# Kernel optimization log

Measured on AMD Instinct MI355X. Metric: run time of the kernel, lower is better.

## Reference

```python
import jax, jax.numpy as jnp
import numpy as np

HEADS = 8


def setup_inputs() -> dict:
    key = jax.random.key(0)
    ks = jax.random.split(key, 18)
    B, L, D, N = 512, 70, 128, 100000
    r = lambda i, shape: jax.random.normal(ks[i], shape, dtype=jnp.float32) * 0.1
    return {
        "hidden": r(0, (B, L, D)),
        "hidden0": r(1, (B, L, D)),
        "mask": jnp.ones((B, L), dtype=jnp.int32),
        "s": r(2, (B, D)),
        "emb": r(3, (N, D)),
        "attn_in_w": r(4, (3 * D, D)),
        "attn_in_b": r(5, (3 * D,)),
        "attn_out_w": r(6, (D, D)),
        "attn_out_b": r(7, (D,)),
        "w_zero": r(8, (D, D)),
        "b_zero": r(9, (D,)),
        "w_one": r(10, (D, D)),
        "b_one": r(11, (D,)),
        "w_two": r(12, (D, D)),
        "b_two": r(13, (D,)),
        "w_three": r(14, (HEADS, D)),
        "w_gate": r(15, (1, 2 * D)),
        "w_trans": r(16, (D, 2 * D)),
        "b_trans": r(17, (D,)),
    }


def _mha(q, k, v, in_w, in_b, out_w, out_b, h):
    # torch.nn.MultiheadAttention, eval mode (dropout=0)
    B, Lq, D = q.shape
    Lk = k.shape[1]
    hd = D // h
    wq, wk, wv = jnp.split(in_w, 3, axis=0)
    bq, bk, bv = jnp.split(in_b, 3)
    qp = (q @ wq.T + bq).reshape(B, Lq, h, hd)
    kp = (k @ wk.T + bk).reshape(B, Lk, h, hd)
    vp = (v @ wv.T + bv).reshape(B, Lk, h, hd)
    scores = jnp.einsum("bqhd,bkhd->bhqk", qp, kp) / jnp.sqrt(jnp.float32(hd))
    w = jax.nn.softmax(scores, axis=-1)
    o = jnp.einsum("bhqk,bkhd->bqhd", w, vp).reshape(B, Lq, D)
    return o @ out_w.T + out_b


def reference(hidden, hidden0, mask, s, emb,
              attn_in_w, attn_in_b, attn_out_w, attn_out_b,
              w_zero, b_zero, w_one, b_one, w_two, b_two,
              w_three, w_gate, w_trans, b_trans):
    B, L, D = hidden.shape
    H = HEADS
    # last-item gather (last_k = 1)
    last_idx = jnp.clip(jnp.sum(mask, axis=1) - 1, 0, 1000)
    ht0 = hidden[jnp.arange(B), last_idx]  # [B, D]
    ht1 = ht0
    # attention of pooled session vector over item states
    ht = _mha(s[:, None, :], hidden, hidden,
              attn_in_w, attn_in_b, attn_out_w, attn_out_b, H)  # [B, 1, D]
    # sigmoid gated fusion of hidden0 / hidden
    sigma = jax.nn.sigmoid(jnp.concatenate([hidden0, hidden], axis=-1) @ w_gate.T)  # [B, L, 1]
    hidden = hidden0 * sigma + hidden * (1.0 - sigma)
    # additive multi-head attention scores
    q0 = (ht1 @ w_zero.T + b_zero)[:, None, :]          # [B, 1, D]
    q1 = ht @ w_one.T + b_one                           # [B, 1, D]
    q2 = hidden @ w_two.T + b_two                       # [B, L, D]
    alpha = jax.nn.sigmoid(q1 + q2 + q0) @ w_three.T    # [B, L, H]
    alpha = jnp.where((mask == 0)[:, :, None], -jnp.inf, alpha)
    alpha = jax.nn.softmax(alpha, axis=1)
    # head-split mask-weighted sum reduction
    mf = mask.astype(hidden.dtype)[:, :, None]
    a = jnp.sum((alpha[..., None] * hidden.reshape(B, L, H, D // H)).reshape(B, L, D) * mf, axis=1)  # [B, D]
    # hybrid transform with last item
    a = jnp.concatenate([a, ht0], axis=1) @ w_trans.T + b_trans
    # normalized scoring against item table (skipping padding idx 0)
    b = emb[1:]
    a = a / (jnp.linalg.norm(a, axis=1, keepdims=True) + 1e-12)
    b = b / (jnp.linalg.norm(b, axis=1, keepdims=True) + 1e-12)
    scores = 12.0 * (a @ b.T)  # [B, n_node-1]
    return scores
```

## Files before the change

### kernel.cpp

```cpp
#include <hip/hip_runtime.h>
#include <hip/hip_bf16.h>

#define B_SZ 512
#define L_SZ 70
#define D_SZ 128
#define NCOL 99999
#define M_ROWS (B_SZ * L_SZ)

typedef __attribute__((ext_vector_type(4))) float f32x4;
typedef __attribute__((ext_vector_type(8))) short bf16x8;

static __device__ __forceinline__ short f2bf(float x) {
    union { float f; unsigned u; } v; v.f = x;
    unsigned r = v.u + 0x7fffu + ((v.u >> 16) & 1u);
    return (short)(r >> 16);
}
static __device__ __forceinline__ float bf2f(unsigned short h) {
    union { unsigned u; float f; } v; v.u = ((unsigned)h) << 16; return v.f;
}

__global__ void k_prep_w(const float* attn_in_w, const float* w_two,
                         short* Wkv, short* W2) {
    int i = blockIdx.x * 256 + threadIdx.x;
    if (i < 256 * 128) Wkv[i] = f2bf(attn_in_w[128 * 128 + i]);
    if (i < 128 * 128) W2[i] = f2bf(w_two[i]);
}

__global__ void k_ht0_qp(const float* hidden, const int* mask, const float* s,
                         const float* attn_in_w, const float* attn_in_b,
                         float* ht0, float* qp) {
    int b = blockIdx.x, t = threadIdx.x;
    __shared__ float s_sh[128];
    __shared__ int idx_sh;
    if (t < 64) {
        int acc = 0;
        for (int l = t; l < L_SZ; l += 64) acc += mask[b * L_SZ + l];
        for (int off = 32; off; off >>= 1) acc += __shfl_down(acc, off);
        if (t == 0) {
            int idx = acc - 1;
            if (idx < 0) idx = 0;
            if (idx > L_SZ - 1) idx = L_SZ - 1;
            idx_sh = idx;
        }
    }
    s_sh[t] = s[b * 128 + t];
    __syncthreads();
    int idx = idx_sh;
    ht0[b * 128 + t] = hidden[(b * L_SZ + idx) * 128 + t];
    float acc = attn_in_b[t];
    const float* wq = attn_in_w + t * 128;
    for (int k = 0; k < 128; k++) acc += s_sh[k] * wq[k];
    qp[b * 128 + t] = acc;
}

__global__ void k_gate(const float* hidden, const float* hidden0,
                       const float* w_gate, short* g_bf) {
    int row = blockIdx.x, t = threadIdx.x;
    float h0 = hidden0[row * 128 + t], h = hidden[row * 128 + t];
    float p = h0 * w_gate[t] + h * w_gate[128 + t];
    for (int off = 32; off; off >>= 1) p += __shfl_down(p, off);
    __shared__ float part[2];
    __shared__ float sig_sh;
    if ((t & 63) == 0) part[t >> 6] = p;
    __syncthreads();
    if (t == 0) {
        float tot = part[0] + part[1];
        sig_sh = 1.f / (1.f + __expf(-tot));
    }
    __syncthreads();
    float sg = sig_sh;
    g_bf[row * 128 + t] = f2bf(h0 * sg + h * (1.f - sg));
}

__global__ void k_gemm_kv(const float* hidden, const short* Wkv,
                          const float* attn_in_b, short* kv) {
    int lane = threadIdx.x & 63, w = threadIdx.x >> 6;
    int r0 = blockIdx.x * 64 + w * 16;
    int ar = r0 + (lane & 15);
    int kbase = (lane >> 4) * 8;
    bf16x8 aF[4];
    const float* Arow = hidden + ar * 128 + kbase;
    for (int kk = 0; kk < 4; kk++) {
        float4 x0 = *(const float4*)(Arow + kk * 32);
        float4 x1 = *(const float4*)(Arow + kk * 32 + 4);
        bf16x8 f;
        f[0] = f2bf(x0.x); f[1] = f2bf(x0.y); f[2] = f2bf(x0.z); f[3] = f2bf(x0.w);
        f[4] = f2bf(x1.x); f[5] = f2bf(x1.y); f[6] = f2bf(x1.z); f[7] = f2bf(x1.w);
        aF[kk] = f;
    }
    int cl = lane & 15;
    int rowbase = r0 + (lane >> 4) * 4;
    for (int ct = 0; ct < 16; ct++) {
        int c = ct * 16 + cl;
        f32x4 acc = {0.f, 0.f, 0.f, 0.f};
        const short* Brow = Wkv + c * 128 + kbase;
        for (int kk = 0; kk < 4; kk++) {
            bf16x8 bF = *(const bf16x8*)(Brow + kk * 32);
            acc = __builtin_amdgcn_mfma_f32_16x16x32_bf16(aF[kk], bF, acc, 0, 0, 0);
        }
        float bias = attn_in_b[128 + c];
        for (int rg = 0; rg < 4; rg++)
            kv[(rowbase + rg) * 256 + c] = f2bf(acc[rg] + bias);
    }
}

__global__ void k_attn(const short* kv, const float* qp, const float* ht0,
                       const float* attn_out_w, const float* attn_out_b,
                       const float* w_zero, const float* b_zero,
                       const float* w_one, const float* b_one, float* q01) {
    int b = blockIdx.x, t = threadIdx.x;
    __shared__ float kp_s[L_SZ][128];
    __shared__ float qp_s[128];
    __shared__ float sc[8][72];
    __shared__ float o_s[128];
    __shared__ float ht_s[128];
    __shared__ float ht0_s[128];
    qp_s[t] = qp[b * 128 + t];
    ht0_s[t] = ht0[b * 128 + t];
    const unsigned short* kvrow = (const unsigned short*)kv + b * L_SZ * 256;
    for (int i = t; i < L_SZ * 128; i += 128) {
        int l = i >> 7, d = i & 127;
        kp_s[l][d] = bf2f(kvrow[l * 256 + d]);
    }
    __syncthreads();
    for (int task = t; task < 8 * L_SZ; task += 128) {
        int h = task / L_SZ, l = task % L_SZ;
        float acc = 0.f;
        for (int j = 0; j < 16; j++) acc += qp_s[h * 16 + j] * kp_s[l][h * 16 + j];
        sc[h][l] = acc * 0.25f;
    }
    __syncthreads();
    if (t < 8) {
        float m = -1e30f;
        for (int l = 0; l < L_SZ; l++) m = fmaxf(m, sc[t][l]);
        float ssum = 0.f;
        for (int l = 0; l < L_SZ; l++) { float e = __expf(sc[t][l] - m); sc[t][l] = e; ssum += e; }
        float inv = 1.f / ssum;
        for (int l = 0; l < L_SZ; l++) sc[t][l] *= inv;
    }
    __syncthreads();
    {
        int h = t >> 4;
        float acc = 0.f;
        for (int l = 0; l < L_SZ; l++) acc += sc[h][l] * bf2f(kvrow[l * 256 + 128 + t]);
        o_s[t] = acc;
    }
    __syncthreads();
    {
        float acc = attn_out_b[t];
        const float* wr = attn_out_w + t * 128;
        for (int k = 0; k < 128; k++) acc += o_s[k] * wr[k];
        ht_s[t] = acc;
    }
    __syncthreads();
    {
        float acc = b_one[t] + b_zero[t];
        const float* w1 = w_one + t * 128;
        const float* w0 = w_zero + t * 128;
        for (int k = 0; k < 128; k++) acc += ht_s[k] * w1[k] + ht0_s[k] * w0[k];
        q01[b * 128 + t] = acc;
    }
}

__global__ void k_gemm_q2_alpha(const short* g_bf, const short* W2, const float* b_two,
                                const float* q01, const float* w_three, float* alphaL) {
    int lane = threadIdx.x & 63, w = threadIdx.x >> 6;
    int r0 = blockIdx.x * 64 + w * 16;
    int ar = r0 + (lane & 15);
    int kbase = (lane >> 4) * 8;
    bf16x8 aF[4];
    const short* Arow = g_bf + ar * 128 + kbase;
    for (int kk = 0; kk < 4; kk++) aF[kk] = *(const bf16x8*)(Arow + kk * 32);
    float part[4][8];
    for (int r = 0; r < 4; r++)
        for (int h = 0; h < 8; h++) part[r][h] = 0.f;
    int cl = lane & 15;
    int rowbase = r0 + (lane >> 4) * 4;
    for (int ct = 0; ct < 8; ct++) {
        int c = ct * 16 + cl;
        f32x4 acc = {0.f, 0.f, 0.f, 0.f};
        const short* Brow = W2 + c * 128 + kbase;
        for (int kk = 0; kk < 4; kk++) {
            bf16x8 bF = *(const bf16x8*)(Brow + kk * 32);
            acc = __builtin_amdgcn_mfma_f32_16x16x32_bf16(aF[kk], bF, acc, 0, 0, 0);
        }
        float bias = b_two[c];
        for (int rg = 0; rg < 4; rg++) {
            int row = rowbase + rg;
            int bb = row / L_SZ;
            float val = acc[rg] + bias + q01[bb * 128 + c];
            float sg = 1.f / (1.f + __expf(-val));
            for (int h = 0; h < 8; h++) part[rg][h] += sg * w_three[h * 128 + c];
        }
    }
    for (int off = 1; off < 16; off <<= 1)
        for (int rg = 0; rg < 4; rg++)
            for (int h = 0; h < 8; h++)
                part[rg][h] += __shfl_xor(part[rg][h], off);
    if ((lane & 15) == 0) {
        for (int rg = 0; rg < 4; rg++) {
            int row = rowbase + rg;
            for (int h = 0; h < 8; h++) alphaL[row * 8 + h] = part[rg][h];
        }
    }
}

__global__ void k_alpha_a(const float* alphaL, const int* mask, const short* g_bf,
                          const float* ht0, const float* w_trans, const float* b_trans,
                          short* a_bf) {
    int b = blockIdx.x, t = threadIdx.x;
    __shared__ float aw[L_SZ][8];
    __shared__ float mf[L_SZ];
    __shared__ float a_s[128];
    __shared__ float ht0_s[128];
    __shared__ float red[2];
    for (int i = t; i < L_SZ; i += 128) mf[i] = (float)mask[b * L_SZ + i];
    for (int i = t; i < L_SZ * 8; i += 128) aw[i >> 3][i & 7] = alphaL[b * L_SZ * 8 + i];
    ht0_s[t] = ht0[b * 128 + t];
    __syncthreads();
    if (t < 8) {
        float m = -1e30f;
        for (int l = 0; l < L_SZ; l++) {
            float v = (mf[l] == 0.f) ? -1e30f : aw[l][t];
            if (v > m) m = v;
        }
        float ssum = 0.f;
        for (int l = 0; l < L_SZ; l++) {
            float v = (mf[l] == 0.f) ? -1e30f : aw[l][t];
            float e = __expf(v - m);
            ssum += e; aw[l][t] = e;
        }
        float inv = 1.f / ssum;
        for (int l = 0; l < L_SZ; l++) aw[l][t] *= inv;
    }
    __syncthreads();
    int h = t >> 4;
    float acc = 0.f;
    const unsigned short* grow = (const unsigned short*)g_bf + b * L_SZ * 128 + t;
    for (int l = 0; l < L_SZ; l++) acc += aw[l][h] * bf2f(grow[l * 128]) * mf[l];
    a_s[t] = acc;
    __syncthreads();
    float a2 = b_trans[t];
    const float* wt = w_trans + t * 256;
    for (int k = 0; k < 128; k++) a2 += a_s[k] * wt[k] + ht0_s[k] * wt[128 + k];
    float sq = a2 * a2;
    for (int off = 32; off; off >>= 1) sq += __shfl_down(sq, off);
    if ((t & 63) == 0) red[t >> 6] = sq;
    __syncthreads();
    float nrm = sqrtf(red[0] + red[1]) + 1e-12f;
    a_bf[b * 128 + t] = f2bf(a2 / nrm);
}

__global__ void k_embnorm(const float* emb, short* bn) {
    int w = threadIdx.x >> 6, lane = threadIdx.x & 63;
    int row = blockIdx.x * 4 + w;
    if (row >= NCOL) return;
    const float* e = emb + (row + 1) * 128;
    float x0 = e[lane], x1 = e[lane + 64];
    float sq = x0 * x0 + x1 * x1;
    for (int off = 32; off; off >>= 1) sq += __shfl_xor(sq, off);
    float inv = 1.f / (sqrtf(sq) + 1e-12f);
    bn[row * 128 + lane] = f2bf(x0 * inv);
    bn[row * 128 + lane + 64] = f2bf(x1 * inv);
}

__global__ void k_final(const short* a_bf, const short* bn, float* out) {
    int lane = threadIdx.x & 63, w = threadIdx.x >> 6;
    int wr = w >> 1, wc = w & 1;
    int rbase = blockIdx.y * 128 + wr * 64;
    int cbase = blockIdx.x * 128 + wc * 64;
    int kbase = (lane >> 4) * 8;
    int rl = lane & 15;
    bf16x8 aF[4][4];
    for (int rt = 0; rt < 4; rt++) {
        const short* Arow = a_bf + (rbase + rt * 16 + rl) * 128 + kbase;
        for (int kk = 0; kk < 4; kk++) aF[rt][kk] = *(const bf16x8*)(Arow + kk * 32);
    }
    f32x4 acc[4][4];
    for (int rt = 0; rt < 4; rt++)
        for (int ct = 0; ct < 4; ct++) acc[rt][ct] = (f32x4){0.f, 0.f, 0.f, 0.f};
    for (int ct = 0; ct < 4; ct++) {
        int c = cbase + ct * 16 + rl;
        bf16x8 bF[4];
        if (c < NCOL) {
            const short* Brow = bn + (long)c * 128 + kbase;
            for (int kk = 0; kk < 4; kk++) bF[kk] = *(const bf16x8*)(Brow + kk * 32);
        } else {
            for (int kk = 0; kk < 4; kk++) bF[kk] = (bf16x8){0, 0, 0, 0, 0, 0, 0, 0};
        }
        for (int kk = 0; kk < 4; kk++)
            for (int rt = 0; rt < 4; rt++)
                acc[rt][ct] = __builtin_amdgcn_mfma_f32_16x16x32_bf16(aF[rt][kk], bF[kk], acc[rt][ct], 0, 0, 0);
    }
    int rowoff = (lane >> 4) * 4;
    for (int rt = 0; rt < 4; rt++) {
        int r = rbase + rt * 16 + rowoff;
        for (int ct = 0; ct < 4; ct++) {
            int c = cbase + ct * 16 + rl;
            if (c >= NCOL) continue;
            for (int rg = 0; rg < 4; rg++)
                out[(long)(r + rg) * NCOL + c] = 12.f * acc[rt][ct][rg];
        }
    }
}

extern "C" void kernel_launch(void* const* d_in, const int* in_sizes, int n_in,
                              void* d_out, int out_size, void* d_ws, size_t ws_size,
                              hipStream_t stream) {
    const float* hidden     = (const float*)d_in[0];
    const float* hidden0    = (const float*)d_in[1];
    const int*   mask       = (const int*)d_in[2];
    const float* s          = (const float*)d_in[3];
    const float* emb        = (const float*)d_in[4];
    const float* attn_in_w  = (const float*)d_in[5];
    const float* attn_in_b  = (const float*)d_in[6];
    const float* attn_out_w = (const float*)d_in[7];
    const float* attn_out_b = (const float*)d_in[8];
    const float* w_zero     = (const float*)d_in[9];
    const float* b_zero     = (const float*)d_in[10];
    const float* w_one      = (const float*)d_in[11];
    const float* b_one      = (const float*)d_in[12];
    const float* w_two      = (const float*)d_in[13];
    const float* b_two      = (const float*)d_in[14];
    const float* w_three    = (const float*)d_in[15];
    const float* w_gate     = (const float*)d_in[16];
    const float* w_trans    = (const float*)d_in[17];
    const float* b_trans    = (const float*)d_in[18];
    float* out = (float*)d_out;

    char* p = (char*)d_ws;
    float* ht0    = (float*)p; p += (size_t)B_SZ * 128 * 4;
    float* qp     = (float*)p; p += (size_t)B_SZ * 128 * 4;
    float* q01    = (float*)p; p += (size_t)B_SZ * 128 * 4;
    float* alphaL = (float*)p; p += (size_t)B_SZ * L_SZ * 8 * 4;
    short* a_bf   = (short*)p; p += (size_t)B_SZ * 128 * 2;
    short* Wkv    = (short*)p; p += (size_t)256 * 128 * 2;
    short* W2     = (short*)p; p += (size_t)128 * 128 * 2;
    short* g_bf   = (short*)p; p += (size_t)M_ROWS * 128 * 2;
    short* kv     = (short*)p; p += (size_t)M_ROWS * 256 * 2;
    short* bn     = (short*)p; p += (size_t)NCOL * 128 * 2;

    k_prep_w<<<128, 256, 0, stream>>>(attn_in_w, w_two, Wkv, W2);
    k_ht0_qp<<<B_SZ, 128, 0, stream>>>(hidden, mask, s, attn_in_w, attn_in_b, ht0, qp);
    k_gate<<<M_ROWS, 128, 0, stream>>>(hidden, hidden0, w_gate, g_bf);
    k_gemm_kv<<<M_ROWS / 64, 256, 0, stream>>>(hidden, Wkv, attn_in_b, kv);
    k_attn<<<B_SZ, 128, 0, stream>>>(kv, qp, ht0, attn_out_w, attn_out_b,
                                     w_zero, b_zero, w_one, b_one, q01);
    k_gemm_q2_alpha<<<M_ROWS / 64, 256, 0, stream>>>(g_bf, W2, b_two, q01, w_three, alphaL);
    k_alpha_a<<<B_SZ, 128, 0, stream>>>(alphaL, mask, g_bf, ht0, w_trans, b_trans, a_bf);
    k_embnorm<<<(NCOL + 3) / 4, 256, 0, stream>>>(emb, bn);
    k_final<<<dim3((NCOL + 127) / 128, 4), 256, 0, stream>>>(a_bf, bn, out);
}
```

Before: 490.6 us.

## Fuse emb normalization into final GEMM, transpose small weights, merge qp into attention

The embedding normalization kernel is folded into the final scoring GEMM. Each block now normalizes its 128 item rows into bf16 register fragments and loops over all 512 batch rows, staging outputs through LDS so the global stores are coalesced. Small fp32 weight matrices are pre-transposed so the per-thread matvec loops read coalesced columns, and the ht0/qp computation moves into the attention kernel, removing two launches and the bn round trip. The trade-off is less grid parallelism in the final kernel (one block per column tile instead of four) and two barriers per row tile.

```diff
diff --git a/kernel.cpp b/kernel.cpp
--- a/kernel.cpp
+++ b/kernel.cpp
@@ -19,38 +19,25 @@
     union { unsigned u; float f; } v; v.u = ((unsigned)h) << 16; return v.f;
 }
 
-__global__ void k_prep_w(const float* attn_in_w, const float* w_two,
-                         short* Wkv, short* W2) {
+__global__ void k_prep(const float* attn_in_w, const float* w_two,
+                       const float* attn_out_w, const float* w_zero,
+                       const float* w_one, const float* w_trans,
+                       short* Wkv, short* W2,
+                       float* wqT, float* woT, float* w0T, float* w1T, float* wtT) {
     int i = blockIdx.x * 256 + threadIdx.x;
     if (i < 256 * 128) Wkv[i] = f2bf(attn_in_w[128 * 128 + i]);
-    if (i < 128 * 128) W2[i] = f2bf(w_two[i]);
-}
-
-__global__ void k_ht0_qp(const float* hidden, const int* mask, const float* s,
-                         const float* attn_in_w, const float* attn_in_b,
-                         float* ht0, float* qp) {
-    int b = blockIdx.x, t = threadIdx.x;
-    __shared__ float s_sh[128];
-    __shared__ int idx_sh;
-    if (t < 64) {
-        int acc = 0;
-        for (int l = t; l < L_SZ; l += 64) acc += mask[b * L_SZ + l];
-        for (int off = 32; off; off >>= 1) acc += __shfl_down(acc, off);
-        if (t == 0) {
-            int idx = acc - 1;
-            if (idx < 0) idx = 0;
-            if (idx > L_SZ - 1) idx = L_SZ - 1;
-            idx_sh = idx;
-        }
-    }
-    s_sh[t] = s[b * 128 + t];
-    __syncthreads();
-    int idx = idx_sh;
-    ht0[b * 128 + t] = hidden[(b * L_SZ + idx) * 128 + t];
-    float acc = attn_in_b[t];
-    const float* wq = attn_in_w + t * 128;
-    for (int k = 0; k < 128; k++) acc += s_sh[k] * wq[k];
-    qp[b * 128 + t] = acc;
+    if (i < 128 * 128) {
+        W2[i] = f2bf(w_two[i]);
+        int r = i >> 7, c = i & 127;
+        wqT[c * 128 + r] = attn_in_w[i];
+        woT[c * 128 + r] = attn_out_w[i];
+        w0T[c * 128 + r] = w_zero[i];
+        w1T[c * 128 + r] = w_one[i];
+    }
+    if (i < 128 * 256) {
+        int r = i >> 8, c = i & 255;
+        wtT[c * 128 + r] = w_trans[i];
+    }
 }
 
 __global__ void k_gate(const float* hidden, const float* hidden0,
@@ -104,23 +91,43 @@
     }
 }
 
-__global__ void k_attn(const short* kv, const float* qp, const float* ht0,
-                       const float* attn_out_w, const float* attn_out_b,
-                       const float* w_zero, const float* b_zero,
-                       const float* w_one, const float* b_one, float* q01) {
+__global__ void k_attn(const float* hidden, const int* mask, const float* s,
+                       const float* wqT, const float* attn_in_b,
+                       const short* kv,
+                       const float* woT, const float* attn_out_b,
+                       const float* w0T, const float* b_zero,
+                       const float* w1T, const float* b_one,
+                       float* ht0, float* q01) {
     int b = blockIdx.x, t = threadIdx.x;
     __shared__ float kp_s[L_SZ][128];
-    __shared__ float qp_s[128];
+    __shared__ float s_sh[128], qp_s[128], o_s[128], ht_s[128], ht0_s[128];
     __shared__ float sc[8][72];
-    __shared__ float o_s[128];
-    __shared__ float ht_s[128];
-    __shared__ float ht0_s[128];
-    qp_s[t] = qp[b * 128 + t];
-    ht0_s[t] = ht0[b * 128 + t];
-    const unsigned short* kvrow = (const unsigned short*)kv + b * L_SZ * 256;
+    __shared__ int idx_sh;
+    if (t < 64) {
+        int acc = 0;
+        for (int l = t; l < L_SZ; l += 64) acc += mask[b * L_SZ + l];
+        for (int off = 32; off; off >>= 1) acc += __shfl_down(acc, off);
+        if (t == 0) {
+            int idx = acc - 1;
+            if (idx < 0) idx = 0;
+            if (idx > L_SZ - 1) idx = L_SZ - 1;
+            idx_sh = idx;
+        }
+    }
+    s_sh[t] = s[b * 128 + t];
+    const unsigned short* kvrow = (const unsigned short*)kv + (size_t)b * L_SZ * 256;
     for (int i = t; i < L_SZ * 128; i += 128) {
         int l = i >> 7, d = i & 127;
         kp_s[l][d] = bf2f(kvrow[l * 256 + d]);
+    }
+    __syncthreads();
+    {
+        float h0 = hidden[((size_t)b * L_SZ + idx_sh) * 128 + t];
+        ht0[b * 128 + t] = h0;
+        ht0_s[t] = h0;
+        float acc = attn_in_b[t];
+        for (int k = 0; k < 128; k++) acc += s_sh[k] * wqT[k * 128 + t];
+        qp_s[t] = acc;
     }
     __syncthreads();
     for (int task = t; task < 8 * L_SZ; task += 128) {
@@ -148,16 +155,13 @@
     __syncthreads();
     {
         float acc = attn_out_b[t];
-        const float* wr = attn_out_w + t * 128;
-        for (int k = 0; k < 128; k++) acc += o_s[k] * wr[k];
+        for (int k = 0; k < 128; k++) acc += o_s[k] * woT[k * 128 + t];
         ht_s[t] = acc;
     }
     __syncthreads();
     {
         float acc = b_one[t] + b_zero[t];
-        const float* w1 = w_one + t * 128;
-        const float* w0 = w_zero + t * 128;
-        for (int k = 0; k < 128; k++) acc += ht_s[k] * w1[k] + ht0_s[k] * w0[k];
+        for (int k = 0; k < 128; k++) acc += ht_s[k] * w1T[k * 128 + t] + ht0_s[k] * w0T[k * 128 + t];
         q01[b * 128 + t] = acc;
     }
 }
@@ -206,7 +210,7 @@
 }
 
 __global__ void k_alpha_a(const float* alphaL, const int* mask, const short* g_bf,
-                          const float* ht0, const float* w_trans, const float* b_trans,
+                          const float* ht0, const float* wtT, const float* b_trans,
                           short* a_bf) {
     int b = blockIdx.x, t = threadIdx.x;
     __shared__ float aw[L_SZ][8];
@@ -241,8 +245,8 @@
     a_s[t] = acc;
     __syncthreads();
     float a2 = b_trans[t];
-    const float* wt = w_trans + t * 256;
-    for (int k = 0; k < 128; k++) a2 += a_s[k] * wt[k] + ht0_s[k] * wt[128 + k];
+    for (int k = 0; k < 128; k++)
+        a2 += a_s[k] * wtT[k * 128 + t] + ht0_s[k] * wtT[(128 + k) * 128 + t];
     float sq = a2 * a2;
     for (int off = 32; off; off >>= 1) sq += __shfl_down(sq, off);
     if ((t & 63) == 0) red[t >> 6] = sq;
@@ -251,55 +255,67 @@
     a_bf[b * 128 + t] = f2bf(a2 / nrm);
 }
 
-__global__ void k_embnorm(const float* emb, short* bn) {
-    int w = threadIdx.x >> 6, lane = threadIdx.x & 63;
-    int row = blockIdx.x * 4 + w;
-    if (row >= NCOL) return;
-    const float* e = emb + (row + 1) * 128;
-    float x0 = e[lane], x1 = e[lane + 64];
-    float sq = x0 * x0 + x1 * x1;
-    for (int off = 32; off; off >>= 1) sq += __shfl_xor(sq, off);
-    float inv = 1.f / (sqrtf(sq) + 1e-12f);
-    bn[row * 128 + lane] = f2bf(x0 * inv);
-    bn[row * 128 + lane + 64] = f2bf(x1 * inv);
-}
-
-__global__ void k_final(const short* a_bf, const short* bn, float* out) {
-    int lane = threadIdx.x & 63, w = threadIdx.x >> 6;
-    int wr = w >> 1, wc = w & 1;
-    int rbase = blockIdx.y * 128 + wr * 64;
-    int cbase = blockIdx.x * 128 + wc * 64;
-    int kbase = (lane >> 4) * 8;
-    int rl = lane & 15;
-    bf16x8 aF[4][4];
-    for (int rt = 0; rt < 4; rt++) {
-        const short* Arow = a_bf + (rbase + rt * 16 + rl) * 128 + kbase;
-        for (int kk = 0; kk < 4; kk++) aF[rt][kk] = *(const bf16x8*)(Arow + kk * 32);
-    }
-    f32x4 acc[4][4];
-    for (int rt = 0; rt < 4; rt++)
-        for (int ct = 0; ct < 4; ct++) acc[rt][ct] = (f32x4){0.f, 0.f, 0.f, 0.f};
-    for (int ct = 0; ct < 4; ct++) {
-        int c = cbase + ct * 16 + rl;
-        bf16x8 bF[4];
-        if (c < NCOL) {
-            const short* Brow = bn + (long)c * 128 + kbase;
-            for (int kk = 0; kk < 4; kk++) bF[kk] = *(const bf16x8*)(Brow + kk * 32);
+__global__ void __launch_bounds__(256, 4) k_final(const short* a_bf, const float* emb, float* out) {
+    __shared__ float lds_c[16][132];
+    int t = threadIdx.x;
+    int lane = t & 63, w = t >> 6;
+    int bx = blockIdx.x;
+    int cl = lane & 15, kg = lane >> 4;
+    int kbase = kg * 8;
+
+    bf16x8 bF[2][4];
+    for (int ct2 = 0; ct2 < 2; ct2++) {
+        int c0 = bx * 128 + w * 32 + ct2 * 16 + cl;
+        float x[4][8];
+        float ss = 0.f;
+        if (c0 < NCOL) {
+            const float* e = emb + (size_t)(c0 + 1) * 128 + kbase;
+            for (int kk = 0; kk < 4; kk++) {
+                float4 v0 = *(const float4*)(e + kk * 32);
+                float4 v1 = *(const float4*)(e + kk * 32 + 4);
+                x[kk][0] = v0.x; x[kk][1] = v0.y; x[kk][2] = v0.z; x[kk][3] = v0.w;
+                x[kk][4] = v1.x; x[kk][5] = v1.y; x[kk][6] = v1.z; x[kk][7] = v1.w;
+                for (int j = 0; j < 8; j++) ss += x[kk][j] * x[kk][j];
+            }
         } else {
-            for (int kk = 0; kk < 4; kk++) bF[kk] = (bf16x8){0, 0, 0, 0, 0, 0, 0, 0};
-        }
-        for (int kk = 0; kk < 4; kk++)
-            for (int rt = 0; rt < 4; rt++)
-                acc[rt][ct] = __builtin_amdgcn_mfma_f32_16x16x32_bf16(aF[rt][kk], bF[kk], acc[rt][ct], 0, 0, 0);
-    }
-    int rowoff = (lane >> 4) * 4;
-    for (int rt = 0; rt < 4; rt++) {
-        int r = rbase + rt * 16 + rowoff;
-        for (int ct = 0; ct < 4; ct++) {
-            int c = cbase + ct * 16 + rl;
-            if (c >= NCOL) continue;
-            for (int rg = 0; rg < 4; rg++)
-                out[(long)(r + rg) * NCOL + c] = 12.f * acc[rt][ct][rg];
+            for (int kk = 0; kk < 4; kk++)
+                for (int j = 0; j < 8; j++) x[kk][j] = 0.f;
+        }
+        ss += __shfl_xor(ss, 16);
+        ss += __shfl_xor(ss, 32);
+        float inv = 1.f / (sqrtf(ss) + 1e-12f);
+        for (int kk = 0; kk < 4; kk++) {
+            bf16x8 f;
+            for (int j = 0; j < 8; j++) f[j] = f2bf(x[kk][j] * inv);
+            bF[ct2][kk] = f;
+        }
+    }
+
+    int cend = NCOL - bx * 128;
+    if (cend > 128) cend = 128;
+
+    for (int rt = 0; rt < 32; rt++) {
+        bf16x8 aF[4];
+        const short* Arow = a_bf + ((size_t)(rt * 16 + cl)) * 128 + kbase;
+        for (int kk = 0; kk < 4; kk++) aF[kk] = *(const bf16x8*)(Arow + kk * 32);
+        f32x4 acc0 = {0.f, 0.f, 0.f, 0.f}, acc1 = {0.f, 0.f, 0.f, 0.f};
+        for (int kk = 0; kk < 4; kk++) {
+            acc0 = __builtin_amdgcn_mfma_f32_16x16x32_bf16(aF[kk], bF[0][kk], acc0, 0, 0, 0);
+            acc1 = __builtin_amdgcn_mfma_f32_16x16x32_bf16(aF[kk], bF[1][kk], acc1, 0, 0, 0);
+        }
+        __syncthreads();
+        for (int rg = 0; rg < 4; rg++) {
+            lds_c[kg * 4 + rg][w * 32 + cl]      = 12.f * acc0[rg];
+            lds_c[kg * 4 + rg][w * 32 + 16 + cl] = 12.f * acc1[rg];
+        }
+        __syncthreads();
+        for (int p = 0; p < 4; p++) {
+            int row = p * 4 + w;
+            size_t gr = (size_t)(rt * 16 + row) * NCOL + (size_t)bx * 128;
+            for (int q = 0; q < 2; q++) {
+                int col = q * 64 + lane;
+                if (col < cend) out[gr + col] = lds_c[row][col];
+            }
         }
     }
 }
@@ -330,24 +346,26 @@
 
     char* p = (char*)d_ws;
     float* ht0    = (float*)p; p += (size_t)B_SZ * 128 * 4;
-    float* qp     = (float*)p; p += (size_t)B_SZ * 128 * 4;
     float* q01    = (float*)p; p += (size_t)B_SZ * 128 * 4;
     float* alphaL = (float*)p; p += (size_t)B_SZ * L_SZ * 8 * 4;
     short* a_bf   = (short*)p; p += (size_t)B_SZ * 128 * 2;
     short* Wkv    = (short*)p; p += (size_t)256 * 128 * 2;
     short* W2     = (short*)p; p += (size_t)128 * 128 * 2;
+    float* wqT    = (float*)p; p += (size_t)128 * 128 * 4;
+    float* woT    = (float*)p; p += (size_t)128 * 128 * 4;
+    float* w0T    = (float*)p; p += (size_t)128 * 128 * 4;
+    float* w1T    = (float*)p; p += (size_t)128 * 128 * 4;
+    float* wtT    = (float*)p; p += (size_t)256 * 128 * 4;
     short* g_bf   = (short*)p; p += (size_t)M_ROWS * 128 * 2;
     short* kv     = (short*)p; p += (size_t)M_ROWS * 256 * 2;
-    short* bn     = (short*)p; p += (size_t)NCOL * 128 * 2;
-
-    k_prep_w<<<128, 256, 0, stream>>>(attn_in_w, w_two, Wkv, W2);
-    k_ht0_qp<<<B_SZ, 128, 0, stream>>>(hidden, mask, s, attn_in_w, attn_in_b, ht0, qp);
+
+    k_prep<<<128, 256, 0, stream>>>(attn_in_w, w_two, attn_out_w, w_zero, w_one, w_trans,
+                                    Wkv, W2, wqT, woT, w0T, w1T, wtT);
     k_gate<<<M_ROWS, 128, 0, stream>>>(hidden, hidden0, w_gate, g_bf);
     k_gemm_kv<<<M_ROWS / 64, 256, 0, stream>>>(hidden, Wkv, attn_in_b, kv);
-    k_attn<<<B_SZ, 128, 0, stream>>>(kv, qp, ht0, attn_out_w, attn_out_b,
-                                     w_zero, b_zero, w_one, b_one, q01);
+    k_attn<<<B_SZ, 128, 0, stream>>>(hidden, mask, s, wqT, attn_in_b, kv,
+                                     woT, attn_out_b, w0T, b_zero, w1T, b_one, ht0, q01);
     k_gemm_q2_alpha<<<M_ROWS / 64, 256, 0, stream>>>(g_bf, W2, b_two, q01, w_three, alphaL);
-    k_alpha_a<<<B_SZ, 128, 0, stream>>>(alphaL, mask, g_bf, ht0, w_trans, b_trans, a_bf);
-    k_embnorm<<<(NCOL + 3) / 4, 256, 0, stream>>>(emb, bn);
-    k_final<<<dim3((NCOL + 127) / 128, 4), 256, 0, stream>>>(a_bf, bn, out);
-}
+    k_alpha_a<<<B_SZ, 128, 0, stream>>>(alphaL, mask, g_bf, ht0, wtT, b_trans, a_bf);
+    k_final<<<(NCOL + 127) / 128, 256, 0, stream>>>(a_bf, emb, out);
+}
```

Measured after the change: 459.5 us. 6.3% less time.
